# Kernel optimization log

Hardware: AMD Instinct MI355X
Metric: run time of the kernel (lower is better)

Reference implementation:

```python
import jax, jax.numpy as jnp
import numpy as np

B, N, C = 64, 320, 768
H = 12
D = C // H  # 64 head dim


def setup_inputs() -> dict:
    key = jax.random.key(0)
    k1, k2, k3, k4, k5 = jax.random.split(key, 5)
    s = 0.02
    return {
        "x": jax.random.normal(k1, (B, N, C), jnp.float32),
        "w_qkv": jax.random.normal(k2, (3 * C, C), jnp.float32) * s,
        "b_qkv": jax.random.normal(k3, (3 * C,), jnp.float32) * s,
        "w_proj": jax.random.normal(k4, (C, C), jnp.float32) * s,
        "b_proj": jax.random.normal(k5, (C,), jnp.float32) * s,
        "num_t": 64,
        "num_s": 256,
    }


def reference(x, w_qkv, b_qkv, w_proj, b_proj, num_t, num_s):
    Bx, Nx, Cx = x.shape
    scale = 1.0 / jnp.sqrt(jnp.asarray(D, x.dtype))
    # qkv projection: [B,N,3C] -> [3,B,H,N,D]
    qkv = x @ w_qkv.T + b_qkv
    qkv = qkv.reshape(Bx, Nx, 3, H, D).transpose(2, 0, 3, 1, 4)
    q, k, v = qkv[0], qkv[1], qkv[2]
    q_t, q_s = q[:, :, :num_t], q[:, :, num_t:]
    k_t = k[:, :, :num_t]
    v_t = v[:, :, :num_t]
    # template self-attention: [B,H,num_t,num_t]
    attn_t = jax.nn.softmax(jnp.einsum("bhqd,bhkd->bhqk", q_t, k_t) * scale, axis=-1)
    x_t = jnp.einsum("bhqk,bhkd->bhqd", attn_t, v_t)
    x_t = x_t.transpose(0, 2, 1, 3).reshape(Bx, num_t, Cx)
    # search attends to all tokens: [B,H,num_s,N]
    attn_s = jax.nn.softmax(jnp.einsum("bhqd,bhkd->bhqk", q_s, k) * scale, axis=-1)
    x_s = jnp.einsum("bhqk,bhkd->bhqd", attn_s, v)
    x_s = x_s.transpose(0, 2, 1, 3).reshape(Bx, num_s, Cx)
    out = jnp.concatenate([x_t, x_s], axis=1)
    return out @ w_proj.T + b_proj
```

## Files before the change

### kernel.cpp

```cpp
#include <hip/hip_runtime.h>
#include <hip/hip_bf16.h>


typedef __attribute__((ext_vector_type(8))) short short8;
typedef __attribute__((ext_vector_type(4))) float f32x4;
typedef __hip_bfloat16 bf16;

#define NTOK 320
#define CDIM 768
#define NHEAD 12
#define MFMA16(a,b,c) __builtin_amdgcn_mfma_f32_16x16x32_bf16((a),(b),(c),0,0,0)

__device__ __forceinline__ unsigned short bfbits(float v) {
    bf16 h = __float2bfloat16(v);
    unsigned short u; __builtin_memcpy(&u, &h, 2);
    return u;
}

__device__ __forceinline__ short8 ldfrag(const bf16* p) { return *(const short8*)p; }
__device__ __forceinline__ short8 ldfrag(const float* p) {
    float4 a = *(const float4*)p;
    float4 b = *(const float4*)(p + 4);
    short8 r;
    r[0]=(short)bfbits(a.x); r[1]=(short)bfbits(a.y); r[2]=(short)bfbits(a.z); r[3]=(short)bfbits(a.w);
    r[4]=(short)bfbits(b.x); r[5]=(short)bfbits(b.y); r[6]=(short)bfbits(b.z); r[7]=(short)bfbits(b.w);
    return r;
}

__device__ __forceinline__ void stage16(const bf16* g, bf16* l) {
    __builtin_amdgcn_global_load_lds(
        (const __attribute__((address_space(1))) void*)g,
        (__attribute__((address_space(3))) void*)l, 16, 0, 0);
}

__global__ __launch_bounds__(256) void cvt3_kernel(const float* __restrict__ s0, bf16* __restrict__ d0, int n0,
                                                   const float* __restrict__ s1, bf16* __restrict__ d1, int n1,
                                                   const float* __restrict__ s2, bf16* __restrict__ d2, int n2)
{
    const int ntot = n0 + n1 + n2;
    int i = blockIdx.x * 256 + threadIdx.x;
    const int stride = gridDim.x * 256;
    for (; i < ntot; i += stride) {
        const float* s; bf16* d; int j = i;
        if (j < n0)              { s = s0; d = d0; }
        else if ((j -= n0) < n1) { s = s1; d = d1; }
        else                     { j -= n1; s = s2; d = d2; }
        const float4 a = ((const float4*)s)[2 * (size_t)j];
        const float4 b = ((const float4*)s)[2 * (size_t)j + 1];
        short8 r;
        r[0]=(short)bfbits(a.x); r[1]=(short)bfbits(a.y); r[2]=(short)bfbits(a.z); r[3]=(short)bfbits(a.w);
        r[4]=(short)bfbits(b.x); r[5]=(short)bfbits(b.y); r[6]=(short)bfbits(b.z); r[7]=(short)bfbits(b.w);
        ((short8*)d)[j] = r;
    }
}

template<int NOUT, int EPI, int BF16B>
__global__ __launch_bounds__(256) void gemm_bt16(const bf16* __restrict__ A,
                                                 const void* __restrict__ Bmv,
                                                 const float* __restrict__ bias,
                                                 void* __restrict__ o0,
                                                 void* __restrict__ o1,
                                                 void* __restrict__ o2)
{
    __shared__ alignas(16) bf16 As[2 * 128 * 32];
    __shared__ alignas(16) bf16 Bs[2 * 128 * 32];
    const int tid  = threadIdx.x;
    const int lane = tid & 63;
    const int wv   = tid >> 6;
    const int r16  = lane & 15;
    const int kg   = lane >> 4;

    constexpr int GX  = NOUT / 128;
    constexpr int NWG = GX * 160;
    int flat = blockIdx.y * GX + blockIdx.x;
    flat = (flat & 7) * (NWG >> 3) + (flat >> 3);
    const int byy = flat / GX;
    const int bxx = flat - byy * GX;
    const int m0  = byy * 128;
    const int n0  = bxx * 128;
    const int wm  = (wv & 1) * 64;
    const int wn  = (wv >> 1) * 64;

    const bf16*  Ab   = A + (size_t)m0 * CDIM;
    const bf16*  Bb16 = (const bf16*)Bmv  + (size_t)n0 * CDIM;
    const float* Bb32 = (const float*)Bmv + (size_t)n0 * CDIM;

    const int ra0 = tid >> 2;
    const int ca0 = (tid & 3) * 8;

    f32x4 acc[4][4] = {};

    if constexpr (BF16B) {
        const bf16* gA0 = Ab   + (size_t)ra0        * CDIM + ca0;
        const bf16* gA1 = Ab   + (size_t)(ra0 + 64) * CDIM + ca0;
        const bf16* gB0 = Bb16 + (size_t)ra0        * CDIM + ca0;
        const bf16* gB1 = Bb16 + (size_t)(ra0 + 64) * CDIM + ca0;

        auto stage = [&](int k0, int buf) {
            const int lb = buf * 4096;
            stage16(gA0 + k0, &As[lb + (size_t)(wv * 64) * 8]);
            stage16(gA1 + k0, &As[lb + (size_t)(wv * 64 + 256) * 8]);
            stage16(gB0 + k0, &Bs[lb + (size_t)(wv * 64) * 8]);
            stage16(gB1 + k0, &Bs[lb + (size_t)(wv * 64 + 256) * 8]);
        };
        auto compute = [&](int buf) {
            const int lb = buf * 4096;
            short8 af[4], bfr[4];
            #pragma unroll
            for (int mt = 0; mt < 4; mt++)
                af[mt] = *(const short8*)&As[lb + (wm + mt * 16 + r16) * 32 + kg * 8];
            #pragma unroll
            for (int nt = 0; nt < 4; nt++)
                bfr[nt] = *(const short8*)&Bs[lb + (wn + nt * 16 + r16) * 32 + kg * 8];
            #pragma unroll
            for (int mt = 0; mt < 4; mt++)
                #pragma unroll
                for (int nt = 0; nt < 4; nt++)
                    acc[mt][nt] = MFMA16(af[mt], bfr[nt], acc[mt][nt]);
        };

        stage(0, 0);
        __syncthreads();
        for (int k0 = 0; k0 < CDIM; k0 += 64) {
            stage(k0 + 32, 1);
            compute(0);
            __syncthreads();
            if (k0 + 64 < CDIM) stage(k0 + 64, 0);
            compute(1);
            __syncthreads();
        }
    } else {
        for (int k0 = 0; k0 < CDIM; k0 += 32) {
            short8 gb0 = ldfrag(Bb32 + (size_t)ra0        * CDIM + k0 + ca0);
            short8 gb1 = ldfrag(Bb32 + (size_t)(ra0 + 64) * CDIM + k0 + ca0);
            __syncthreads();
            stage16(Ab + (size_t)ra0        * CDIM + k0 + ca0, &As[(size_t)(wv * 64) * 8]);
            stage16(Ab + (size_t)(ra0 + 64) * CDIM + k0 + ca0, &As[(size_t)(wv * 64 + 256) * 8]);
            *(short8*)&Bs[(size_t)tid * 8]         = gb0;
            *(short8*)&Bs[(size_t)(tid + 256) * 8] = gb1;
            __syncthreads();

            short8 af[4], bfr[4];
            #pragma unroll
            for (int mt = 0; mt < 4; mt++)
                af[mt] = *(const short8*)&As[(wm + mt * 16 + r16) * 32 + kg * 8];
            #pragma unroll
            for (int nt = 0; nt < 4; nt++)
                bfr[nt] = *(const short8*)&Bs[(wn + nt * 16 + r16) * 32 + kg * 8];
            #pragma unroll
            for (int mt = 0; mt < 4; mt++)
                #pragma unroll
                for (int nt = 0; nt < 4; nt++)
                    acc[mt][nt] = MFMA16(af[mt], bfr[nt], acc[mt][nt]);
        }
    }

    #pragma unroll
    for (int nt = 0; nt < 4; nt++) {
        const int gn = n0 + wn + nt * 16 + r16;
        const float bv = bias[gn];
        if (EPI == 0) {
            const int which = gn / CDIM;
            const int rem   = gn - which * CDIM;
            const int hh    = rem >> 6;
            const int dd    = rem & 63;
            #pragma unroll
            for (int mt = 0; mt < 4; mt++) {
                const int gm0  = m0 + wm + mt * 16 + kg * 4;
                const int bidx = gm0 / NTOK;
                const int nn0  = gm0 - bidx * NTOK;
                float v[4];
                #pragma unroll
                for (int r = 0; r < 4; r++) v[r] = acc[mt][nt][r] + bv;
                if (which == 0) {
                    bf16* q = (bf16*)o0 + ((size_t)(bidx * NHEAD + hh) * NTOK + nn0) * 64 + dd;
                    #pragma unroll
                    for (int r = 0; r < 4; r++) q[(size_t)r * 64] = __float2bfloat16(v[r]);
                } else if (which == 1) {
                    bf16* k = (bf16*)o1 + ((size_t)(bidx * NHEAD + hh) * NTOK + nn0) * 64 + dd;
                    #pragma unroll
                    for (int r = 0; r < 4; r++) k[(size_t)r * 64] = __float2bfloat16(v[r]);
                } else {
                    ushort4 p;
                    unsigned short* ps = (unsigned short*)&p;
                    #pragma unroll
                    for (int r = 0; r < 4; r++) ps[r] = bfbits(v[r]);
                    *(ushort4*)((bf16*)o2 + ((size_t)(bidx * NHEAD + hh) * 64 + dd) * NTOK + nn0) = p;
                }
            }
        } else {
            float* out = (float*)o0;
            #pragma unroll
            for (int mt = 0; mt < 4; mt++) {
                const int gm0 = m0 + wm + mt * 16 + kg * 4;
                #pragma unroll
                for (int r = 0; r < 4; r++)
                    out[(size_t)(gm0 + r) * NOUT + gn] = acc[mt][nt][r] + bv;
            }
        }
    }
}

#define ATTN_NWG (768 * 10)
__global__ __launch_bounds__(256, 4) void attn_kernel(const bf16* __restrict__ q_ws,
                                                      const bf16* __restrict__ k_ws,
                                                      const bf16* __restrict__ vt_ws,
                                                      bf16* __restrict__ attn,
                                                      const int* __restrict__ numt_p)
{
    __shared__ alignas(16) float S[32 * 320];
    int num_t = 64;
    if (numt_p) {
        int v = *numt_p;
        float f = __int_as_float(v);
        if (v >= 1 && v <= 319) num_t = v;
        else if (f >= 1.f && f <= 319.f) num_t = (int)f;
    }
    if (num_t <= 0 || num_t > NTOK || (num_t & 31)) num_t = 64;

    const int tid  = threadIdx.x;
    const int lane = tid & 63;
    const int w    = tid >> 6;
    const int r16  = lane & 15;
    const int kg   = lane >> 4;

    int blk = blockIdx.x;
    blk = (blk & 7) * (ATTN_NWG / 8) + (blk >> 3);
    const int bh  = blk / 10;
    const int qt  = blk - bh * 10;
    const int b   = bh / NHEAD;
    const int h   = bh - b * NHEAD;
    const int q0  = qt * 32;
    const int nk  = (q0 + 32 <= num_t) ? num_t : NTOK;
    const int nk16 = nk >> 4;

    const bf16* qp = q_ws  + (size_t)bh * NTOK * 64;
    const bf16* kp = k_ws  + (size_t)bh * NTOK * 64;
    const bf16* vp = vt_ws + (size_t)bh * 64 * NTOK;

    short8 qf[2][2];
    #pragma unroll
    for (int ks = 0; ks < 2; ks++)
        #pragma unroll
        for (int mt = 0; mt < 2; mt++)
            qf[ks][mt] = ldfrag(qp + (size_t)(q0 + mt * 16 + r16) * 64 + ks * 32 + kg * 8);

    const float scale = 0.125f;
    auto p1body = [&](int nt) {
        f32x4 a0 = {}, a1 = {};
        #pragma unroll
        for (int ks = 0; ks < 2; ks++) {
            short8 kf = ldfrag(kp + (size_t)(nt * 16 + r16) * 64 + ks * 32 + kg * 8);
            a0 = MFMA16(qf[ks][0], kf, a0);
            a1 = MFMA16(qf[ks][1], kf, a1);
        }
        const int col = nt * 16 + r16;
        #pragma unroll
        for (int r = 0; r < 4; r++) {
            const int ro  = kg * 4 + r;
            const int swz = (ro & 7) << 2;
            S[ro * 320        + (col ^ swz)] = a0[r] * scale;
            S[(16 + ro) * 320 + (col ^ swz)] = a1[r] * scale;
        }
    };
    if (nk16 == 20) {
        #pragma unroll
        for (int it = 0; it < 5; it++) p1body(w + it * 4);
    } else {
        for (int nt = w; nt < nk16; nt += 4) p1body(nt);
    }
    __syncthreads();

    {
        const int row = tid >> 3;
        const int sub = tid & 7;
        const int swzw = (row & 7) << 2;
        const int swzh = (row & 7) << 3;
        float* Sr = S + row * 320;
        bf16*  Pr = (bf16*)Sr;
        float mx = -1e30f;
        for (int c = sub * 4; c < nk; c += 32) {
            float4 t = *(float4*)&Sr[c ^ swzw];
            mx = fmaxf(mx, fmaxf(fmaxf(t.x, t.y), fmaxf(t.z, t.w)));
        }
        #pragma unroll
        for (int m = 1; m < 8; m <<= 1) mx = fmaxf(mx, __shfl_xor(mx, m));
        float sum = 0.f;
        for (int c = sub * 4; c < nk; c += 32) {
            float4 t = *(float4*)&Sr[c ^ swzw];
            t.x = __expf(t.x - mx); t.y = __expf(t.y - mx);
            t.z = __expf(t.z - mx); t.w = __expf(t.w - mx);
            sum += t.x + t.y + t.z + t.w;
            ushort4 p;
            p.x = bfbits(t.x); p.y = bfbits(t.y); p.z = bfbits(t.z); p.w = bfbits(t.w);
            *(ushort4*)&Pr[c ^ swzh] = p;
        }
        #pragma unroll
        for (int m = 1; m < 8; m <<= 1) sum += __shfl_xor(sum, m);
        if (sub == 0) Sr[316 ^ swzw] = 1.0f / sum;
    }
    __syncthreads();

    const int mt  = w & 1;
    const int ntb = w >> 1;
    const int prow = mt * 16 + r16;
    const bf16* Pbr = (const bf16*)(S + prow * 320);
    const int pswzh = (prow & 7) << 3;
    f32x4 o[2] = {};
    auto p3body = [&](int ks) {
        short8 af = *(const short8*)&Pbr[(ks * 32 + kg * 8) ^ pswzh];
        #pragma unroll
        for (int i = 0; i < 2; i++) {
            const int nt = ntb + i * 2;
            short8 vf = ldfrag(vp + (size_t)(nt * 16 + r16) * NTOK + ks * 32 + kg * 8);
            o[i] = MFMA16(af, vf, o[i]);
        }
    };
    if (nk == NTOK) {
        #pragma unroll
        for (int ks = 0; ks < 10; ks++) p3body(ks);
    } else {
        for (int ks = 0; ks < (nk >> 5); ks++) p3body(ks);
    }
    #pragma unroll
    for (int i = 0; i < 2; i++) {
        const int nt = ntb + i * 2;
        const int dd = nt * 16 + r16;
        #pragma unroll
        for (int r = 0; r < 4; r++) {
            const int qrow  = mt * 16 + kg * 4 + r;
            const float invs = S[qrow * 320 + (316 ^ ((qrow & 7) << 2))];
            const float val = o[i][r] * invs;
            const int token = q0 + qrow;
            attn[(((size_t)b * NTOK + token) * NHEAD + h) * 64 + dd] = __float2bfloat16(val);
        }
    }
}

extern "C" void kernel_launch(void* const* d_in, const int* in_sizes, int n_in,
                              void* d_out, int out_size, void* d_ws, size_t ws_size,
                              hipStream_t stream)
{
    float* out = (float*)d_out;

    const float *x = nullptr, *w_qkv = nullptr, *b_qkv = nullptr,
                *w_proj = nullptr, *b_proj = nullptr;
    const int* numt_p = nullptr;
    for (int i = 0; i < n_in; i++) {
        switch (in_sizes[i]) {
            case 15728640: x      = (const float*)d_in[i]; break;
            case 1769472:  w_qkv  = (const float*)d_in[i]; break;
            case 2304:     b_qkv  = (const float*)d_in[i]; break;
            case 589824:   w_proj = (const float*)d_in[i]; break;
            case 768:      b_proj = (const float*)d_in[i]; break;
            case 1:        if (!numt_p) numt_p = (const int*)d_in[i]; break;
            default: break;
        }
    }
    if (!x || !w_qkv || !b_qkv || !w_proj || !b_proj) return;

    const size_t per      = (size_t)64 * NHEAD * NTOK * 64;
    const size_t wq_elems = (size_t)2304 * 768;
    const size_t wp_elems = (size_t)768 * 768;
    const size_t base_need = 4 * per * sizeof(bf16);
    const size_t full_need = base_need + (wq_elems + wp_elems) * sizeof(bf16);
    if (ws_size < base_need) return;
    const bool full = ws_size >= full_need;

    bf16* q_ws  = (bf16*)d_ws;
    bf16* k_ws  = q_ws  + per;
    bf16* vt_ws = k_ws  + per;
    bf16* attn  = vt_ws + per;
    bf16* x16   = attn;
    bf16* wq16  = attn + per;
    bf16* wp16  = wq16 + wq_elems;

    if (full)
        cvt3_kernel<<<2048, 256, 0, stream>>>(x, x16, (int)(per / 8),
                                              w_qkv, wq16, (int)(wq_elems / 8),
                                              w_proj, wp16, (int)(wp_elems / 8));
    else
        cvt3_kernel<<<2048, 256, 0, stream>>>(x, x16, (int)(per / 8),
                                              x, x16, 0, x, x16, 0);

    if (full)
        gemm_bt16<2304, 0, 1><<<dim3(18, 160), 256, 0, stream>>>(
            x16, wq16, b_qkv, q_ws, k_ws, vt_ws);
    else
        gemm_bt16<2304, 0, 0><<<dim3(18, 160), 256, 0, stream>>>(
            x16, w_qkv, b_qkv, q_ws, k_ws, vt_ws);

    attn_kernel<<<ATTN_NWG, 256, 0, stream>>>(q_ws, k_ws, vt_ws, attn, numt_p);

    if (full)
        gemm_bt16<768, 1, 1><<<dim3(6, 160), 256, 0, stream>>>(
            attn, wp16, b_proj, out, nullptr, nullptr);
    else
        gemm_bt16<768, 1, 0><<<dim3(6, 160), 256, 0, stream>>>(
            attn, w_proj, b_proj, out, nullptr, nullptr);
}
```

Measured before the change: 389.0 us.

## Triple-buffer bf16 GEMM staging with swizzled LDS and one barrier per k-tile

The bf16 GEMM path moves from a double buffer with two barriers per 64-wide step to a three-stage LDS ring. It uses explicit vmcnt waits and a single barrier per 32-wide k-tile, so global loads run two tiles ahead of compute. The LDS column is XOR-swizzled on both the staging and fragment-read sides to cut bank conflicts, and MFMA blocks are wrapped in s_setprio. LDS use rises by half, which may lower occupancy, and correctness depends on stage16 issuing exactly the expected number of vector memory ops for the vmcnt(4) wait.

```diff
diff --git a/kernel.cpp b/kernel.cpp
--- a/kernel.cpp
+++ b/kernel.cpp
@@ -62,8 +62,8 @@
                                                  void* __restrict__ o1,
                                                  void* __restrict__ o2)
 {
-    __shared__ alignas(16) bf16 As[2 * 128 * 32];
-    __shared__ alignas(16) bf16 Bs[2 * 128 * 32];
+    __shared__ alignas(16) bf16 As[3 * 4096];
+    __shared__ alignas(16) bf16 Bs[3 * 4096];
     const int tid  = threadIdx.x;
     const int lane = tid & 63;
     const int wv   = tid >> 6;
@@ -86,50 +86,54 @@
     const float* Bb32 = (const float*)Bmv + (size_t)n0 * CDIM;
 
     const int ra0 = tid >> 2;
-    const int ca0 = (tid & 3) * 8;
 
     f32x4 acc[4][4] = {};
 
     if constexpr (BF16B) {
-        const bf16* gA0 = Ab   + (size_t)ra0        * CDIM + ca0;
-        const bf16* gA1 = Ab   + (size_t)(ra0 + 64) * CDIM + ca0;
-        const bf16* gB0 = Bb16 + (size_t)ra0        * CDIM + ca0;
-        const bf16* gB1 = Bb16 + (size_t)(ra0 + 64) * CDIM + ca0;
-
-        auto stage = [&](int k0, int buf) {
-            const int lb = buf * 4096;
-            stage16(gA0 + k0, &As[lb + (size_t)(wv * 64) * 8]);
-            stage16(gA1 + k0, &As[lb + (size_t)(wv * 64 + 256) * 8]);
-            stage16(gB0 + k0, &Bs[lb + (size_t)(wv * 64) * 8]);
-            stage16(gB1 + k0, &Bs[lb + (size_t)(wv * 64 + 256) * 8]);
+        const int ca_sw = (((tid & 3) ^ ((tid >> 3) & 3)) * 8);
+        const bf16* gA0 = Ab   + (size_t)ra0 * CDIM + ca_sw;
+        const bf16* gB0 = Bb16 + (size_t)ra0 * CDIM + ca_sw;
+        const int kgs = (kg ^ ((r16 >> 1) & 3)) * 8;
+
+        auto stage = [&](int kt, int buf) {
+            const int k0 = kt * 32;
+            const size_t lb = (size_t)buf * 4096;
+            stage16(gA0 + k0,             &As[lb + wv * 512]);
+            stage16(gA0 + 64 * CDIM + k0, &As[lb + wv * 512 + 2048]);
+            stage16(gB0 + k0,             &Bs[lb + wv * 512]);
+            stage16(gB0 + 64 * CDIM + k0, &Bs[lb + wv * 512 + 2048]);
         };
         auto compute = [&](int buf) {
-            const int lb = buf * 4096;
+            const size_t lb = (size_t)buf * 4096;
             short8 af[4], bfr[4];
             #pragma unroll
             for (int mt = 0; mt < 4; mt++)
-                af[mt] = *(const short8*)&As[lb + (wm + mt * 16 + r16) * 32 + kg * 8];
+                af[mt] = *(const short8*)&As[lb + (wm + mt * 16 + r16) * 32 + kgs];
             #pragma unroll
             for (int nt = 0; nt < 4; nt++)
-                bfr[nt] = *(const short8*)&Bs[lb + (wn + nt * 16 + r16) * 32 + kg * 8];
+                bfr[nt] = *(const short8*)&Bs[lb + (wn + nt * 16 + r16) * 32 + kgs];
+            __builtin_amdgcn_s_setprio(1);
             #pragma unroll
             for (int mt = 0; mt < 4; mt++)
                 #pragma unroll
                 for (int nt = 0; nt < 4; nt++)
                     acc[mt][nt] = MFMA16(af[mt], bfr[nt], acc[mt][nt]);
+            __builtin_amdgcn_s_setprio(0);
         };
 
+        constexpr int NKT = CDIM / 32;
         stage(0, 0);
-        __syncthreads();
-        for (int k0 = 0; k0 < CDIM; k0 += 64) {
-            stage(k0 + 32, 1);
-            compute(0);
-            __syncthreads();
-            if (k0 + 64 < CDIM) stage(k0 + 64, 0);
-            compute(1);
-            __syncthreads();
+        stage(1, 1);
+        for (int t = 0; t < NKT; ++t) {
+            if (t < NKT - 1) { asm volatile("s_waitcnt vmcnt(4)" ::: "memory"); }
+            else             { asm volatile("s_waitcnt vmcnt(0)" ::: "memory"); }
+            __builtin_amdgcn_s_barrier();
+            asm volatile("" ::: "memory");
+            if (t + 2 < NKT) stage(t + 2, (t + 2) % 3);
+            compute(t % 3);
         }
     } else {
+        const int ca0 = (tid & 3) * 8;
         for (int k0 = 0; k0 < CDIM; k0 += 32) {
             short8 gb0 = ldfrag(Bb32 + (size_t)ra0        * CDIM + k0 + ca0);
             short8 gb1 = ldfrag(Bb32 + (size_t)(ra0 + 64) * CDIM + k0 + ca0);
@@ -166,7 +170,7 @@
             const int dd    = rem & 63;
             #pragma unroll
             for (int mt = 0; mt < 4; mt++) {
-                const int gm0  = m0 + wm + mt * 16 + kg * 4;
+                const int gm0  = m0 + wm + mt * 16 + (lane >> 4) * 4;
                 const int bidx = gm0 / NTOK;
                 const int nn0  = gm0 - bidx * NTOK;
                 float v[4];
@@ -192,7 +196,7 @@
             float* out = (float*)o0;
             #pragma unroll
             for (int mt = 0; mt < 4; mt++) {
-                const int gm0 = m0 + wm + mt * 16 + kg * 4;
+                const int gm0 = m0 + wm + mt * 16 + (lane >> 4) * 4;
                 #pragma unroll
                 for (int r = 0; r < 4; r++)
                     out[(size_t)(gm0 + r) * NOUT + gn] = acc[mt][nt][r] + bv;
```

Result: no change. 389.8 us (+0.2%).
